# Optimization experiments

Measured on AMD Instinct MI355X. Metric: run time of the kernel, lower is better.

The kernel has to match this reference:

```python
import jax, jax.numpy as jnp
import numpy as np

N_POINTS = 1 << 20
N_LEVELS = 16
F_PER_LVL = 2
LOG2_T = 19
T = 1 << LOG2_T
BASE_RES = 16
PER_LEVEL_SCALE = float(np.exp2(np.log2(2048.0 / 16.0) / (N_LEVELS - 1)))
# 8 trilinear corner offsets [8,3]
OFFSETS = np.stack(np.meshgrid(*([np.array([0, 1])] * 3), indexing='ij'), axis=-1).reshape(8, 3)
PRIMES = np.array([1, 2654435761, 805459861], dtype=np.uint32)  # tcnn spatial hash primes


def _level_params(l):
    # tcnn: grid_scale = 2^(l*log2(s)) * base - 1 ; resolution = ceil(scale)+1
    scale = np.exp2(l * np.log2(PER_LEVEL_SCALE)) * BASE_RES - 1.0
    res = int(np.ceil(scale)) + 1
    return float(scale), res


def hash_encode(x, table):
    """x: [N,3] in [0,1]; table: [L,T,F]. Returns [N, L*F]."""
    offs = jnp.asarray(OFFSETS)                     # [8,3] int32
    primes = jnp.asarray(PRIMES)                    # [3] uint32
    feats = []
    for l in range(N_LEVELS):
        scale, res = _level_params(l)
        pos = x * scale + 0.5                       # [N,3]
        pos_grid = jnp.floor(pos)
        w = pos - pos_grid                          # [N,3] interp weights
        c0 = pos_grid.astype(jnp.int32)             # [N,3]
        corners = c0[None, :, :] + offs[:, None, :]  # [8,N,3]
        if res ** 3 <= T:
            # dense indexing for coarse levels (fits in hashmap)
            cc = jnp.clip(corners, 0, res - 1)
            idx = cc[..., 0] + cc[..., 1] * res + cc[..., 2] * (res * res)
        else:
            cu = corners.astype(jnp.uint32)
            h = (cu[..., 0] * primes[0]) ^ (cu[..., 1] * primes[1]) ^ (cu[..., 2] * primes[2])
            idx = (h & jnp.uint32(T - 1)).astype(jnp.int32)
        f = table[l][idx]                           # [8,N,F] gather
        # trilinear weights: prod over dims of (w if corner bit else 1-w)
        wc = jnp.prod(jnp.where(offs[:, None, :] == 1, w[None], 1.0 - w[None]), axis=-1)  # [8,N]
        feats.append(jnp.sum(wc[..., None] * f, axis=0))  # [N,F]
    return jnp.concatenate(feats, axis=-1)          # [N, 32]


def _softplus10(z):
    return jax.nn.softplus(10.0 * z) / 10.0


def setup_inputs() -> dict:
    key = jax.random.key(0)
    k = jax.random.split(key, 6)
    x = jax.random.uniform(k[0], (N_POINTS, 3), dtype=jnp.float32)
    table = jax.random.normal(k[1], (N_LEVELS, T, F_PER_LVL), dtype=jnp.float32) * 1e-2
    w1 = jax.random.normal(k[2], (64, 32), dtype=jnp.float32) * 0.1
    w2 = jax.random.normal(k[3], (64, 64), dtype=jnp.float32) * 0.1
    w3 = jax.random.normal(k[4], (64, 64), dtype=jnp.float32) * 0.1
    w4 = jax.random.normal(k[5], (1, 64), dtype=jnp.float32) * 0.1
    return {"x": x, "table": table, "w1": w1, "w2": w2, "w3": w3, "w4": w4}


def reference(x, table, w1, w2, w3, w4):
    enc = hash_encode(x, table)                     # [N,32]
    h = _softplus10(enc @ w1.T)
    h = _softplus10(h @ w2.T)
    h = _softplus10(h @ w3.T)
    sdf = h @ w4.T                                  # [N,1]
    return sdf
```

## Files before the change

kernel.cpp:

```cpp
#include <hip/hip_runtime.h>
#include <cmath>

#define T_SIZE (1u << 19)

typedef _Float16 h8 __attribute__((ext_vector_type(8)));
typedef _Float16 h4 __attribute__((ext_vector_type(4)));
typedef _Float16 h2 __attribute__((ext_vector_type(2)));
typedef float f4 __attribute__((ext_vector_type(4)));

struct Levels {
    float scale[16];
    int   res[16];
    unsigned dense_mask;
};

__device__ __forceinline__ float softplus10(float z) {
    float e = __builtin_amdgcn_exp2f(fminf(z * 14.426950408889634f, 126.0f));
    return __builtin_amdgcn_logf(1.0f + e) * 0.069314718055994531f;
}

__global__ __launch_bounds__(256) void convert_kernel(
    const float2* __restrict__ t, h2* __restrict__ o, int total4,
    const float* __restrict__ w1, const float* __restrict__ w2,
    const float* __restrict__ w3, _Float16* __restrict__ wh)
{
    int i = blockIdx.x * 256 + threadIdx.x;
    if (i < total4) {
        const float2* src = t + (size_t)i * 4;
        h8 r;
#pragma unroll
        for (int j = 0; j < 4; ++j) {
            float2 v = src[j];
            r[2 * j]     = (_Float16)v.x;
            r[2 * j + 1] = (_Float16)v.y;
        }
        *(h8*)(o + (size_t)i * 4) = r;
    } else {
        int k = i - total4;
        if (k < 10240) {
            float v = (k < 2048) ? w1[k] : (k < 6144) ? w2[k - 2048] : w3[k - 6144];
            wh[k] = (_Float16)v;
        }
    }
}

__device__ __forceinline__ void gather_pair(
    const h2* __restrict__ tl, unsigned i0, unsigned i1,
    float2& v0, float2& v1)
{
    unsigned g = i0 & ~3u;
    union { h8 v; uint4 u; } cv;
    cv.v = *(const h8*)(tl + g);
    unsigned p0 = i0 & 3u;
    unsigned a01 = (p0 & 1u) ? cv.u.y : cv.u.x;
    unsigned a23 = (p0 & 1u) ? cv.u.w : cv.u.z;
    unsigned e0  = (p0 & 2u) ? a23 : a01;
    unsigned e1;
    if ((i1 & ~3u) == g) {
        unsigned p1 = i1 & 3u;
        unsigned b01 = (p1 & 1u) ? cv.u.y : cv.u.x;
        unsigned b23 = (p1 & 1u) ? cv.u.w : cv.u.z;
        e1 = (p1 & 2u) ? b23 : b01;
    } else {
        e1 = *(const unsigned*)(tl + i1);
    }
    h2 c0 = __builtin_bit_cast(h2, e0);
    h2 c1 = __builtin_bit_cast(h2, e1);
    v0 = make_float2((float)c0[0], (float)c0[1]);
    v1 = make_float2((float)c1[0], (float)c1[1]);
}

__device__ __forceinline__ h2 encode_point(
    float px, float py, float pz, float s, int res, bool dense,
    const h2* __restrict__ tl)
{
    float fx = px * s + 0.5f, fy = py * s + 0.5f, fz = pz * s + 0.5f;
    float gx = floorf(fx), gy = floorf(fy), gz = floorf(fz);
    float wx = fx - gx, wy = fy - gy, wz = fz - gz;
    int cx = (int)gx, cy = (int)gy, cz = (int)gz;

    float2 vx0[4], vx1[4];
    if (dense) {
        int r1 = res - 1;
        int x0 = min(cx, r1), x1 = min(cx + 1, r1);
        int y0 = min(cy, r1), y1 = min(cy + 1, r1);
        int z0 = min(cz, r1), z1 = min(cz + 1, r1);
        int rr = res * res;
        int bases[4] = {y0 * res + z0 * rr, y0 * res + z1 * rr,
                        y1 * res + z0 * rr, y1 * res + z1 * rr};
#pragma unroll
        for (int j = 0; j < 4; ++j)
            gather_pair(tl, (unsigned)(x0 + bases[j]), (unsigned)(x1 + bases[j]),
                        vx0[j], vx1[j]);
    } else {
        unsigned hy0 = (unsigned)cy * 2654435761u, hy1 = (unsigned)(cy + 1) * 2654435761u;
        unsigned hz0 = (unsigned)cz * 805459861u,  hz1 = (unsigned)(cz + 1) * 805459861u;
        unsigned Y[4] = {hy0 ^ hz0, hy0 ^ hz1, hy1 ^ hz0, hy1 ^ hz1};
        const unsigned M = T_SIZE - 1;
#pragma unroll
        for (int j = 0; j < 4; ++j)
            gather_pair(tl, ((unsigned)cx ^ Y[j]) & M,
                        ((unsigned)(cx + 1) ^ Y[j]) & M, vx0[j], vx1[j]);
    }

    float wx0 = 1.f - wx, wy0 = 1.f - wy, wz0 = 1.f - wz;
    float wyz[4] = {wy0 * wz0, wy0 * wz, wy * wz0, wy * wz};
    float f0 = 0.f, f1 = 0.f;
#pragma unroll
    for (int j = 0; j < 4; ++j) {
        float w0 = wx0 * wyz[j], w1 = wx * wyz[j];
        f0 += w0 * vx0[j].x + w1 * vx1[j].x;
        f1 += w0 * vx0[j].y + w1 * vx1[j].y;
    }
    h2 r; r[0] = (_Float16)f0; r[1] = (_Float16)f1;
    return r;
}

__global__ __launch_bounds__(256) void encode_kernel(
    const float* __restrict__ xs, const h2* __restrict__ table,
    h2* __restrict__ enc2, Levels lv, int lbase, int N)
{
    __shared__ float sx[768];
    const int i0 = blockIdx.x * 256;
    for (int t = threadIdx.x; t < 768; t += 256) sx[t] = xs[(size_t)i0 * 3 + t];
    __syncthreads();

    const int l = lbase + blockIdx.y;
    const int i = i0 + threadIdx.x;
    if (i >= N) return;
    h2 r = encode_point(sx[threadIdx.x * 3], sx[threadIdx.x * 3 + 1],
                        sx[threadIdx.x * 3 + 2], lv.scale[l], lv.res[l],
                        (lv.dense_mask >> l) & 1u, table + (size_t)l * T_SIZE);
    enc2[(size_t)l * N + i] = r;
}

template <typename WT>
__device__ __forceinline__ h8 load_frag8(const WT* p) {
    if constexpr (sizeof(WT) == 2) {
        return *(const h8*)p;
    } else {
        h8 r;
#pragma unroll
        for (int j = 0; j < 8; ++j) r[j] = (_Float16)p[j];
        return r;
    }
}

template <typename WT, bool LOCAL>
__global__ __launch_bounds__(256, 3) void fused_kernel(
    const float* __restrict__ xs, const h2* __restrict__ table16,
    const h2* __restrict__ enc2,
    const WT* __restrict__ w1, const WT* __restrict__ w2,
    const WT* __restrict__ w3, const float* __restrict__ w4,
    float* __restrict__ out, Levels lv, int N)
{
    constexpr int AR = 72;
    __shared__ __align__(16) char smem[4 * 9216];
    __shared__ float sx[768];

    const int tid  = threadIdx.x;
    const int wave = tid >> 6;
    const int lane = tid & 63;
    const int lrow = lane & 15;
    const int quad = lane >> 4;
    const int base = blockIdx.x * 256;
    char* wmem = smem + wave * 9216;
    const f4 zero = {0.f, 0.f, 0.f, 0.f};

    for (int t = tid; t < 768; t += 256) sx[t] = xs[(size_t)base * 3 + t];
    __syncthreads();
    const float px = sx[tid * 3], py = sx[tid * 3 + 1], pz = sx[tid * 3 + 2];
    const int p = tid & 63;

    if (LOCAL) {
#pragma unroll
        for (int l = 5; l < 15; ++l) {
            h2 v = enc2[(size_t)l * N + base + tid];
            *(h2*)(wmem + ((l >> 2) << 10) + (p << 4) + ((l & 3) << 2)) = v;
        }
        const int LMAP[6] = {0, 1, 2, 3, 4, 15};
#pragma unroll 2
        for (int s6 = 0; s6 < 6; ++s6) {
            const int l = LMAP[s6];
            h2 v = encode_point(px, py, pz, lv.scale[l], lv.res[l],
                                (lv.dense_mask >> l) & 1u,
                                table16 + (size_t)l * T_SIZE);
            *(h2*)(wmem + ((l >> 2) << 10) + (p << 4) + ((l & 3) << 2)) = v;
        }
    } else {
#pragma unroll
        for (int l = 0; l < 16; ++l) {
            h2 v = enc2[(size_t)l * N + base + tid];
            *(h2*)(wmem + ((l >> 2) << 10) + (p << 4) + ((l & 3) << 2)) = v;
        }
    }

    asm volatile("" ::: "memory");

    h8 aW1[4];
#pragma unroll
    for (int tm = 0; tm < 4; ++tm)
        aW1[tm] = load_frag8(w1 + (tm * 16 + lrow) * 32 + quad * 8);
    h8 aW2[4][2], aW3[4][2];
#pragma unroll
    for (int tm = 0; tm < 4; ++tm)
#pragma unroll
        for (int km = 0; km < 2; ++km) {
            aW2[tm][km] = load_frag8(w2 + (tm * 16 + lrow) * 64 + km * 32 + quad * 8);
            aW3[tm][km] = load_frag8(w3 + (tm * 16 + lrow) * 64 + km * 32 + quad * 8);
        }
    h4 w4q[4];
#pragma unroll
    for (int tm = 0; tm < 4; ++tm)
#pragma unroll
        for (int r = 0; r < 4; ++r) w4q[tm][r] = (_Float16)w4[tm * 16 + quad * 4 + r];

    h8 bin[4];
#pragma unroll
    for (int t = 0; t < 4; ++t)
        bin[t] = *(const h8*)(wmem + (quad << 10) + ((t * 16 + lrow) << 4));

    _Float16* wAct = (_Float16*)wmem;

#pragma unroll
    for (int t = 0; t < 4; ++t) {
        const int arow = (t * 16 + lrow) * AR;
#pragma unroll
        for (int tm = 0; tm < 4; ++tm) {
            f4 acc = __builtin_amdgcn_mfma_f32_16x16x32_f16(aW1[tm], bin[t], zero, 0, 0, 0);
            h4 pk;
#pragma unroll
            for (int r = 0; r < 4; ++r) pk[r] = (_Float16)softplus10(acc[r]);
            *(h4*)&wAct[arow + tm * 16 + quad * 4] = pk;
        }
    }

#pragma unroll
    for (int t = 0; t < 4; ++t) {
        const int arow = (t * 16 + lrow) * AR;
        h8 b0 = *(const h8*)&wAct[arow + quad * 8];
        h8 b1 = *(const h8*)&wAct[arow + 32 + quad * 8];
        f4 accs[4];
#pragma unroll
        for (int tm = 0; tm < 4; ++tm) {
            f4 acc = __builtin_amdgcn_mfma_f32_16x16x32_f16(aW2[tm][0], b0, zero, 0, 0, 0);
            acc     = __builtin_amdgcn_mfma_f32_16x16x32_f16(aW2[tm][1], b1, acc,  0, 0, 0);
            accs[tm] = acc;
        }
#pragma unroll
        for (int tm = 0; tm < 4; ++tm) {
            h4 pk;
#pragma unroll
            for (int r = 0; r < 4; ++r) pk[r] = (_Float16)softplus10(accs[tm][r]);
            *(h4*)&wAct[arow + tm * 16 + quad * 4] = pk;
        }
    }

#pragma unroll
    for (int t = 0; t < 4; ++t) {
        const int arow = (t * 16 + lrow) * AR;
        h8 b0 = *(const h8*)&wAct[arow + quad * 8];
        h8 b1 = *(const h8*)&wAct[arow + 32 + quad * 8];
        float sum = 0.f;
#pragma unroll
        for (int tm = 0; tm < 4; ++tm) {
            f4 acc = __builtin_amdgcn_mfma_f32_16x16x32_f16(aW3[tm][0], b0, zero, 0, 0, 0);
            acc     = __builtin_amdgcn_mfma_f32_16x16x32_f16(aW3[tm][1], b1, acc,  0, 0, 0);
#pragma unroll
            for (int r = 0; r < 4; ++r)
                sum += (float)w4q[tm][r] * softplus10(acc[r]);
        }
        sum += __shfl_xor(sum, 16, 64);
        sum += __shfl_xor(sum, 32, 64);
        if (quad == 0)
            out[base + wave * 64 + t * 16 + lrow] = sum;
    }
}

__global__ __launch_bounds__(256) void encode_kernel_f32(
    const float* __restrict__ xs, const float2* __restrict__ table,
    h2* __restrict__ enc2, Levels lv, int N)
{
    const int i = blockIdx.x * 256 + threadIdx.x;
    const int l = blockIdx.y;
    if (i >= N) return;
    float px = xs[3 * i], py = xs[3 * i + 1], pz = xs[3 * i + 2];
    float s = lv.scale[l];
    int res = lv.res[l];
    float fx = px * s + 0.5f, fy = py * s + 0.5f, fz = pz * s + 0.5f;
    float gx = floorf(fx), gy = floorf(fy), gz = floorf(fz);
    float wx = fx - gx, wy = fy - gy, wz = fz - gz;
    int cx = (int)gx, cy = (int)gy, cz = (int)gz;
    unsigned idx[8];
    if ((lv.dense_mask >> l) & 1u) {
        int r1 = res - 1;
        int x0 = min(cx, r1), x1 = min(cx + 1, r1);
        int y0 = min(cy, r1), y1 = min(cy + 1, r1);
        int z0 = min(cz, r1), z1 = min(cz + 1, r1);
        int rr = res * res;
        idx[0] = x0 + y0 * res + z0 * rr; idx[1] = x0 + y0 * res + z1 * rr;
        idx[2] = x0 + y1 * res + z0 * rr; idx[3] = x0 + y1 * res + z1 * rr;
        idx[4] = x1 + y0 * res + z0 * rr; idx[5] = x1 + y0 * res + z1 * rr;
        idx[6] = x1 + y1 * res + z0 * rr; idx[7] = x1 + y1 * res + z1 * rr;
    } else {
        unsigned hx0 = (unsigned)cx, hx1 = (unsigned)(cx + 1);
        unsigned hy0 = (unsigned)cy * 2654435761u, hy1 = (unsigned)(cy + 1) * 2654435761u;
        unsigned hz0 = (unsigned)cz * 805459861u,  hz1 = (unsigned)(cz + 1) * 805459861u;
        idx[0] = (hx0^hy0^hz0) & (T_SIZE-1); idx[1] = (hx0^hy0^hz1) & (T_SIZE-1);
        idx[2] = (hx0^hy1^hz0) & (T_SIZE-1); idx[3] = (hx0^hy1^hz1) & (T_SIZE-1);
        idx[4] = (hx1^hy0^hz0) & (T_SIZE-1); idx[5] = (hx1^hy0^hz1) & (T_SIZE-1);
        idx[6] = (hx1^hy1^hz0) & (T_SIZE-1); idx[7] = (hx1^hy1^hz1) & (T_SIZE-1);
    }
    const float2* tl = table + (size_t)l * T_SIZE;
    float wx0 = 1.f - wx, wy0 = 1.f - wy, wz0 = 1.f - wz;
    float wcs[8] = {wx0*wy0*wz0, wx0*wy0*wz, wx0*wy*wz0, wx0*wy*wz,
                    wx*wy0*wz0,  wx*wy0*wz,  wx*wy*wz0,  wx*wy*wz};
    float f0 = 0.f, f1 = 0.f;
#pragma unroll
    for (int c = 0; c < 8; ++c) {
        float2 v = tl[idx[c]];
        f0 += wcs[c] * v.x; f1 += wcs[c] * v.y;
    }
    h2 r; r[0] = (_Float16)f0; r[1] = (_Float16)f1;
    enc2[(size_t)l * N + i] = r;
}

extern "C" void kernel_launch(void* const* d_in, const int* in_sizes, int n_in,
                              void* d_out, int out_size, void* d_ws, size_t ws_size,
                              hipStream_t stream) {
    const float* x     = (const float*)d_in[0];
    const float* table = (const float*)d_in[1];
    const float* w1    = (const float*)d_in[2];
    const float* w2    = (const float*)d_in[3];
    const float* w3    = (const float*)d_in[4];
    const float* w4    = (const float*)d_in[5];
    float* out = (float*)d_out;
    const int N = in_sizes[0] / 3;

    Levels lv;
    lv.dense_mask = 0;
    const double pls = exp2(log2(2048.0 / 16.0) / 15.0);
    const double lg  = log2(pls);
    for (int l = 0; l < 16; ++l) {
        double sc = exp2((double)l * lg) * 16.0 - 1.0;
        int res = (int)ceil(sc) + 1;
        lv.scale[l] = (float)sc;
        lv.res[l]   = res;
        if ((long long)res * res * res <= (long long)T_SIZE) lv.dense_mask |= (1u << l);
    }

    const size_t encBytes   = (size_t)16 * N * 4;
    const size_t tableBytes = (size_t)16 * T_SIZE * 4;
    const size_t whBytes    = 32768;
    h2* enc2 = (h2*)d_ws;

    const int ptBlocks = (N + 255) / 256;

    if (ws_size >= encBytes + tableBytes + whBytes) {
        h2* table16 = (h2*)((char*)d_ws + encBytes);
        _Float16* wh = (_Float16*)((char*)d_ws + encBytes + tableBytes);
        const int total4 = 16 * T_SIZE / 4;
        const int convBlocks = (total4 + 10240 + 255) / 256;
        hipLaunchKernelGGL(convert_kernel, dim3(convBlocks), dim3(256), 0, stream,
                           (const float2*)table, table16, total4, w1, w2, w3, wh);
        hipLaunchKernelGGL(encode_kernel, dim3(ptBlocks, 10), dim3(256), 0, stream,
                           x, (const h2*)table16, enc2, lv, 5, N);
        hipLaunchKernelGGL((fused_kernel<_Float16, true>), dim3(ptBlocks), dim3(256),
                           0, stream, x, (const h2*)table16, (const h2*)enc2,
                           wh, wh + 2048, wh + 6144, w4, out, lv, N);
    } else {
        hipLaunchKernelGGL(encode_kernel_f32, dim3(ptBlocks, 16), dim3(256), 0, stream,
                           x, (const float2*)table, enc2, lv, N);
        hipLaunchKernelGGL((fused_kernel<float, false>), dim3(ptBlocks), dim3(256),
                           0, stream, x, (const h2*)nullptr, (const h2*)enc2,
                           w1, w2, w3, w4, out, lv, N);
    }
}
```

Measured before the change: 431.5 us.

## Sort points by Morton key before encoding to improve hash-table gather locality

Adds a counting sort of the input points by a 15-bit Morton code (zero bins, histogram with atomics, single-block scan, scatter) into a float4 buffer that carries the original index. The encode and fused MLP kernels then read points in spatially coherent order, and results are scattered back to the original positions. The aim is better cache locality for the table gathers on the dense and coarse levels. In exchange it adds four extra launches, atomics, a serial single-block scan and scattered output writes. Fine hashed levels stay essentially random, so it benefits only part of the gather traffic.

```diff
diff --git a/kernel.cpp b/kernel.cpp
--- a/kernel.cpp
+++ b/kernel.cpp
@@ -2,6 +2,7 @@
 #include <cmath>
 
 #define T_SIZE (1u << 19)
+#define NBINS 32768
 
 typedef _Float16 h8 __attribute__((ext_vector_type(8)));
 typedef _Float16 h4 __attribute__((ext_vector_type(4)));
@@ -42,6 +43,69 @@
             wh[k] = (_Float16)v;
         }
     }
+}
+
+__device__ __forceinline__ unsigned spread3(unsigned v) {
+    v &= 1023u;
+    v = (v | (v << 16)) & 0x030000FFu;
+    v = (v | (v << 8))  & 0x0300F00Fu;
+    v = (v | (v << 4))  & 0x030C30C3u;
+    v = (v | (v << 2))  & 0x09249249u;
+    return v;
+}
+
+__device__ __forceinline__ unsigned morton_key(float px, float py, float pz) {
+    unsigned qx = (unsigned)fminf(fmaxf(px, 0.f) * 32.f, 31.f);
+    unsigned qy = (unsigned)fminf(fmaxf(py, 0.f) * 32.f, 31.f);
+    unsigned qz = (unsigned)fminf(fmaxf(pz, 0.f) * 32.f, 31.f);
+    return (spread3(qx) << 2) | (spread3(qy) << 1) | spread3(qz);
+}
+
+__global__ __launch_bounds__(256) void zero_bins_kernel(unsigned* __restrict__ bins) {
+    bins[blockIdx.x * 256 + threadIdx.x] = 0u;
+}
+
+__global__ __launch_bounds__(256) void hist_kernel(
+    const float* __restrict__ xs, unsigned* __restrict__ bins, int N)
+{
+    int i = blockIdx.x * 256 + threadIdx.x;
+    if (i >= N) return;
+    unsigned k = morton_key(xs[3 * i], xs[3 * i + 1], xs[3 * i + 2]);
+    atomicAdd(&bins[k], 1u);
+}
+
+__global__ __launch_bounds__(1024) void scan_kernel(
+    const unsigned* __restrict__ bins, unsigned* __restrict__ cursor)
+{
+    __shared__ unsigned tmp[1024];
+    const int t = threadIdx.x;
+    unsigned loc[32];
+    unsigned s = 0;
+#pragma unroll
+    for (int j = 0; j < 32; ++j) { loc[j] = s; s += bins[t * 32 + j]; }
+    tmp[t] = s;
+    __syncthreads();
+    for (int d = 1; d < 1024; d <<= 1) {
+        unsigned v = (t >= d) ? tmp[t - d] : 0u;
+        __syncthreads();
+        tmp[t] += v;
+        __syncthreads();
+    }
+    unsigned base = (t > 0) ? tmp[t - 1] : 0u;
+#pragma unroll
+    for (int j = 0; j < 32; ++j) cursor[t * 32 + j] = base + loc[j];
+}
+
+__global__ __launch_bounds__(256) void scatter_kernel(
+    const float* __restrict__ xs, float4* __restrict__ sx4,
+    unsigned* __restrict__ cursor, int N)
+{
+    int i = blockIdx.x * 256 + threadIdx.x;
+    if (i >= N) return;
+    float px = xs[3 * i], py = xs[3 * i + 1], pz = xs[3 * i + 2];
+    unsigned k = morton_key(px, py, pz);
+    unsigned pos = atomicAdd(&cursor[k], 1u);
+    sx4[pos] = make_float4(px, py, pz, __uint_as_float((unsigned)i));
 }
 
 __device__ __forceinline__ void gather_pair(
@@ -134,6 +198,19 @@
     enc2[(size_t)l * N + i] = r;
 }
 
+__global__ __launch_bounds__(256) void encode_kernel_sorted(
+    const float4* __restrict__ xs4, const h2* __restrict__ table,
+    h2* __restrict__ enc2, Levels lv, int lbase, int N)
+{
+    const int i = blockIdx.x * 256 + threadIdx.x;
+    if (i >= N) return;
+    const int l = lbase + blockIdx.y;
+    float4 q = xs4[i];
+    h2 r = encode_point(q.x, q.y, q.z, lv.scale[l], lv.res[l],
+                        (lv.dense_mask >> l) & 1u, table + (size_t)l * T_SIZE);
+    enc2[(size_t)l * N + i] = r;
+}
+
 template <typename WT>
 __device__ __forceinline__ h8 load_frag8(const WT* p) {
     if constexpr (sizeof(WT) == 2) {
@@ -146,10 +223,10 @@
     }
 }
 
-template <typename WT, bool LOCAL>
+template <typename WT, bool LOCAL, bool SORTED>
 __global__ __launch_bounds__(256, 3) void fused_kernel(
-    const float* __restrict__ xs, const h2* __restrict__ table16,
-    const h2* __restrict__ enc2,
+    const float* __restrict__ xs, const float4* __restrict__ xs4,
+    const h2* __restrict__ table16, const h2* __restrict__ enc2,
     const WT* __restrict__ w1, const WT* __restrict__ w2,
     const WT* __restrict__ w3, const float* __restrict__ w4,
     float* __restrict__ out, Levels lv, int N)
@@ -167,9 +244,17 @@
     char* wmem = smem + wave * 9216;
     const f4 zero = {0.f, 0.f, 0.f, 0.f};
 
-    for (int t = tid; t < 768; t += 256) sx[t] = xs[(size_t)base * 3 + t];
-    __syncthreads();
-    const float px = sx[tid * 3], py = sx[tid * 3 + 1], pz = sx[tid * 3 + 2];
+    float px, py, pz;
+    unsigned oi = 0;
+    if constexpr (SORTED) {
+        float4 q = xs4[base + tid];
+        px = q.x; py = q.y; pz = q.z;
+        oi = __float_as_uint(q.w);
+    } else {
+        for (int t = tid; t < 768; t += 256) sx[t] = xs[(size_t)base * 3 + t];
+        __syncthreads();
+        px = sx[tid * 3]; py = sx[tid * 3 + 1]; pz = sx[tid * 3 + 2];
+    }
     const int p = tid & 63;
 
     if (LOCAL) {
@@ -272,8 +357,13 @@
         }
         sum += __shfl_xor(sum, 16, 64);
         sum += __shfl_xor(sum, 32, 64);
-        if (quad == 0)
-            out[base + wave * 64 + t * 16 + lrow] = sum;
+        if constexpr (SORTED) {
+            unsigned t_oi = __shfl(oi, t * 16 + lrow, 64);
+            if (quad == 0) out[t_oi] = sum;
+        } else {
+            if (quad == 0)
+                out[base + wave * 64 + t * 16 + lrow] = sum;
+        }
     }
 }
 
@@ -352,11 +442,36 @@
     const size_t encBytes   = (size_t)16 * N * 4;
     const size_t tableBytes = (size_t)16 * T_SIZE * 4;
     const size_t whBytes    = 32768;
+    const size_t sx4Bytes   = (size_t)N * 16;
+    const size_t binBytes   = (size_t)NBINS * 4 * 2;
     h2* enc2 = (h2*)d_ws;
 
     const int ptBlocks = (N + 255) / 256;
 
-    if (ws_size >= encBytes + tableBytes + whBytes) {
+    if (ws_size >= encBytes + tableBytes + whBytes + sx4Bytes + binBytes) {
+        h2* table16    = (h2*)((char*)d_ws + encBytes);
+        _Float16* wh   = (_Float16*)((char*)d_ws + encBytes + tableBytes);
+        float4* sx4    = (float4*)((char*)d_ws + encBytes + tableBytes + whBytes);
+        unsigned* bins = (unsigned*)((char*)d_ws + encBytes + tableBytes + whBytes + sx4Bytes);
+        unsigned* curs = bins + NBINS;
+
+        const int total4 = 16 * T_SIZE / 4;
+        const int convBlocks = (total4 + 10240 + 255) / 256;
+        hipLaunchKernelGGL(convert_kernel, dim3(convBlocks), dim3(256), 0, stream,
+                           (const float2*)table, table16, total4, w1, w2, w3, wh);
+
+        hipLaunchKernelGGL(zero_bins_kernel, dim3(NBINS / 256), dim3(256), 0, stream, bins);
+        hipLaunchKernelGGL(hist_kernel, dim3(ptBlocks), dim3(256), 0, stream, x, bins, N);
+        hipLaunchKernelGGL(scan_kernel, dim3(1), dim3(1024), 0, stream, bins, curs);
+        hipLaunchKernelGGL(scatter_kernel, dim3(ptBlocks), dim3(256), 0, stream,
+                           x, sx4, curs, N);
+
+        hipLaunchKernelGGL(encode_kernel_sorted, dim3(ptBlocks, 10), dim3(256), 0, stream,
+                           (const float4*)sx4, (const h2*)table16, enc2, lv, 5, N);
+        hipLaunchKernelGGL((fused_kernel<_Float16, true, true>), dim3(ptBlocks), dim3(256),
+                           0, stream, x, (const float4*)sx4, (const h2*)table16,
+                           (const h2*)enc2, wh, wh + 2048, wh + 6144, w4, out, lv, N);
+    } else if (ws_size >= encBytes + tableBytes + whBytes) {
         h2* table16 = (h2*)((char*)d_ws + encBytes);
         _Float16* wh = (_Float16*)((char*)d_ws + encBytes + tableBytes);
         const int total4 = 16 * T_SIZE / 4;
@@ -365,14 +480,14 @@
                            (const float2*)table, table16, total4, w1, w2, w3, wh);
         hipLaunchKernelGGL(encode_kernel, dim3(ptBlocks, 10), dim3(256), 0, stream,
                            x, (const h2*)table16, enc2, lv, 5, N);
-        hipLaunchKernelGGL((fused_kernel<_Float16, true>), dim3(ptBlocks), dim3(256),
-                           0, stream, x, (const h2*)table16, (const h2*)enc2,
-                           wh, wh + 2048, wh + 6144, w4, out, lv, N);
+        hipLaunchKernelGGL((fused_kernel<_Float16, true, false>), dim3(ptBlocks), dim3(256),
+                           0, stream, x, (const float4*)nullptr, (const h2*)table16,
+                           (const h2*)enc2, wh, wh + 2048, wh + 6144, w4, out, lv, N);
     } else {
         hipLaunchKernelGGL(encode_kernel_f32, dim3(ptBlocks, 16), dim3(256), 0, stream,
                            x, (const float2*)table, enc2, lv, N);
-        hipLaunchKernelGGL((fused_kernel<float, false>), dim3(ptBlocks), dim3(256),
-                           0, stream, x, (const h2*)nullptr, (const h2*)enc2,
-                           w1, w2, w3, w4, out, lv, N);
-    }
-}
+        hipLaunchKernelGGL((fused_kernel<float, false, false>), dim3(ptBlocks), dim3(256),
+                           0, stream, x, (const float4*)nullptr, (const h2*)nullptr,
+                           (const h2*)enc2, w1, w2, w3, w4, out, lv, N);
+    }
+}
```

Measured after the change: 491.8 us. 1.14x slower.
